# Kernel optimization log

Measured on AMD Instinct MI355X. Metric: run time of the kernel, lower is better.

## Reference

```python
import jax, jax.numpy as jnp
import numpy as np


def setup_inputs() -> dict:
    key = jax.random.key(0)
    ks = jax.random.split(key, 4)
    T, B, E = 2048, 2, 1024
    query = jax.random.normal(ks[0], (T, B, E), dtype=jnp.float32)
    attn_mask = jnp.zeros((T, T), dtype=jnp.float32)
    Wqkv = jax.random.normal(ks[1], (3 * E, E), dtype=jnp.float32) * 0.02
    bqkv = jnp.zeros((3 * E,), dtype=jnp.float32)
    Wout = jax.random.normal(ks[2], (E, E), dtype=jnp.float32) * 0.02
    bout = jnp.zeros((E,), dtype=jnp.float32)
    return {"query": query, "attn_mask": attn_mask, "Wqkv": Wqkv,
            "bqkv": bqkv, "Wout": Wout, "bout": bout, "num_heads": 16}


def reference(query, attn_mask, Wqkv, bqkv, Wout, bout, num_heads):
    T, B, E = query.shape
    H = num_heads
    hd = E // H
    scaling = hd ** -0.5
    # fused QKV projection: [T,B,3E]
    qkv = jnp.einsum('tbe,fe->tbf', query, Wqkv) + bqkv
    q, k, v = jnp.split(qkv, 3, axis=-1)
    q = q * scaling
    # [T,B,E] -> [B*H, T, hd]
    def to_heads(x):
        return x.reshape(T, B * H, hd).transpose(1, 0, 2)
    q, k, v = to_heads(q), to_heads(k), to_heads(v)
    # scores [B*H, T, T]
    scores = jnp.einsum('bth,bsh->bts', q, k) + attn_mask[None, :, :]
    probs = jax.nn.softmax(scores, axis=-1)  # dropout p=0
    attn = jnp.einsum('bts,bsh->bth', probs, v)  # [B*H, T, hd]
    attn = attn.transpose(1, 0, 2).reshape(T, B, E)
    out = jnp.einsum('tbe,fe->tbf', attn, Wout) + bout
    avg_w = probs.reshape(B, H, T, T).sum(axis=1) / H
    return out, avg_w
```

## Files before the change

### kernel.cpp

```cpp
#include <hip/hip_runtime.h>
#include <cstdint>
#include <cstddef>

#define Tt 2048
#define Bb 2
#define Ee 1024
#define Hh 16
#define HD 64
#define BHh (Bb*Hh)
#define Mm (Tt*Bb)

typedef short bf16x8 __attribute__((ext_vector_type(8)));
typedef float f32x4  __attribute__((ext_vector_type(4)));

#define MFMA16(a,b,c) __builtin_amdgcn_mfma_f32_16x16x32_bf16(a, b, c, 0, 0, 0)

__device__ __forceinline__ unsigned short f2bf(float f) {
    unsigned int u = __builtin_bit_cast(unsigned int, f);
    u += 0x7FFFu + ((u >> 16) & 1u);
    return (unsigned short)(u >> 16);
}
__device__ __forceinline__ unsigned int pack2bf(float lo, float hi) {
    return (unsigned int)f2bf(lo) | ((unsigned int)f2bf(hi) << 16);
}

__device__ __forceinline__ int swzA(int row, int dwcol) {
    return (row*32 + dwcol) ^ ((row & 7) << 2);
}
__device__ __forceinline__ int swzG(int row, int dwcol) {
    return (row*16 + dwcol) ^ ((row & 3) << 2);
}

__device__ __forceinline__ bf16x8 ldfrag(const unsigned short* base, int row, int col) {
    const unsigned int* p = (const unsigned int*)(base + row*66 + col);
    const unsigned int* q = (const unsigned int*)(base + row*66 + col + 16);
    uint4 u;
    u.x = p[0]; u.y = p[1];
    u.z = q[0]; u.w = q[1];
    return __builtin_bit_cast(bf16x8, u);
}

__global__ __launch_bounds__(256)
void to_bf16(const float* __restrict__ src, unsigned short* __restrict__ dst, int n8)
{
    const int stride = gridDim.x * 256;
    for (int i = blockIdx.x*256 + threadIdx.x; i < n8; i += stride) {
        const float4 a = ((const float4*)src)[2*i];
        const float4 b = ((const float4*)src)[2*i + 1];
        const uint4 u = {pack2bf(a.x,a.y), pack2bf(a.z,a.w),
                         pack2bf(b.x,b.y), pack2bf(b.z,b.w)};
        ((uint4*)dst)[i] = u;
    }
}

template<int MODE>
__global__ __launch_bounds__(256)
void gemm_mfma(const unsigned short* __restrict__ A, const unsigned short* __restrict__ W,
               const float* __restrict__ bias, float* __restrict__ Cout,
               unsigned short* __restrict__ qbuf, unsigned short* __restrict__ kbuf,
               unsigned short* __restrict__ vbuf, int N, int K)
{
    __shared__ __align__(16) unsigned int AsDW[2][128*16];
    __shared__ __align__(16) unsigned int WsDW[2][128*16];
    const int tid  = threadIdx.x;
    const int bm   = blockIdx.y * 128;
    const int bn   = blockIdx.x * 128;
    const int w    = tid >> 6;
    const int lane = tid & 63;
    const int lr   = lane & 15;
    const int lg   = lane >> 4;
    const int wm   = (w >> 1) * 64;
    const int wn   = (w & 1) * 64;

    f32x4 acc[4][4];
#pragma unroll
    for (int m = 0; m < 4; ++m)
#pragma unroll
        for (int n = 0; n < 4; ++n)
            acc[m][n] = f32x4{0.f, 0.f, 0.f, 0.f};

    const int r1  = tid >> 2;
    const int cdw = (tid & 3) * 4;

    {
        const uint4 a0 = *(const uint4*)&A[(size_t)(bm + r1)      * K + cdw*2];
        const uint4 a1 = *(const uint4*)&A[(size_t)(bm + r1 + 64) * K + cdw*2];
        const uint4 w0 = *(const uint4*)&W[(size_t)(bn + r1)      * K + cdw*2];
        const uint4 w1 = *(const uint4*)&W[(size_t)(bn + r1 + 64) * K + cdw*2];
        *(uint4*)(AsDW[0] + swzG(r1,      cdw)) = a0;
        *(uint4*)(AsDW[0] + swzG(r1 + 64, cdw)) = a1;
        *(uint4*)(WsDW[0] + swzG(r1,      cdw)) = w0;
        *(uint4*)(WsDW[0] + swzG(r1 + 64, cdw)) = w1;
        __syncthreads();
    }

    int cur = 0;
    for (int k0 = 0; k0 < K; k0 += 32) {
        const bool has_next = (k0 + 32 < K);
        uint4 an0, an1, wn0, wn1;
        if (has_next) {
            an0 = *(const uint4*)&A[(size_t)(bm + r1)      * K + k0 + 32 + cdw*2];
            an1 = *(const uint4*)&A[(size_t)(bm + r1 + 64) * K + k0 + 32 + cdw*2];
            wn0 = *(const uint4*)&W[(size_t)(bn + r1)      * K + k0 + 32 + cdw*2];
            wn1 = *(const uint4*)&W[(size_t)(bn + r1 + 64) * K + k0 + 32 + cdw*2];
        }

        const unsigned int* Ac = AsDW[cur];
        const unsigned int* Wc = WsDW[cur];
        bf16x8 af[4], wf[4];
#pragma unroll
        for (int i = 0; i < 4; ++i) {
            af[i] = __builtin_bit_cast(bf16x8, *(const uint4*)(Ac + swzG(wm + 16*i + lr, 4*lg)));
            wf[i] = __builtin_bit_cast(bf16x8, *(const uint4*)(Wc + swzG(wn + 16*i + lr, 4*lg)));
        }
#pragma unroll
        for (int m = 0; m < 4; ++m)
#pragma unroll
            for (int n = 0; n < 4; ++n)
                acc[m][n] = MFMA16(af[m], wf[n], acc[m][n]);

        if (has_next) {
            *(uint4*)(AsDW[cur ^ 1] + swzG(r1,      cdw)) = an0;
            *(uint4*)(AsDW[cur ^ 1] + swzG(r1 + 64, cdw)) = an1;
            *(uint4*)(WsDW[cur ^ 1] + swzG(r1,      cdw)) = wn0;
            *(uint4*)(WsDW[cur ^ 1] + swzG(r1 + 64, cdw)) = wn1;
        }
        __syncthreads();
        cur ^= 1;
    }

#pragma unroll
    for (int nsub = 0; nsub < 4; ++nsub) {
        const int n0 = bn + wn + 16*nsub + lr;
        const float bv = bias[n0];
#pragma unroll
        for (int msub = 0; msub < 4; ++msub) {
#pragma unroll
            for (int reg = 0; reg < 4; ++reg) {
                const int m = bm + wm + 16*msub + 4*lg + reg;
                float v = acc[msub][nsub][reg] + bv;
                if (MODE == 0) {
                    const int which = n0 >> 10;
                    const int e0 = n0 & 1023;
                    const int h = e0 >> 6, d0 = e0 & 63;
                    if (which == 0) v *= 0.125f;
                    unsigned short* dst = (which == 0) ? qbuf : (which == 1) ? kbuf : vbuf;
                    dst[((size_t)((m & 1)*Hh + h) * Tt + (m >> 1)) * HD + d0] = f2bf(v);
                } else {
                    Cout[(size_t)m * N + n0] = v;
                }
            }
        }
    }
}

__global__ __launch_bounds__(512)
void attn_mfma(const unsigned short* __restrict__ qb, const unsigned short* __restrict__ kb,
               const unsigned short* __restrict__ vb, const float* __restrict__ mask,
               unsigned short* __restrict__ attnb, float* __restrict__ lbuf)
{
    __shared__ __align__(16) unsigned int KsDW[2][64*32];
    __shared__ __align__(16) unsigned short Vt[2][64*66];
    __shared__ float l_sh[128];

    const int tid  = threadIdx.x;
    const int bid  = blockIdx.x;
    const int wid  = (bid & 7) * 64 + (bid >> 3);
    const int bh   = wid & 31;
    const int t0   = (wid >> 5) * 128;
    const int w    = tid >> 6;
    const int lane = tid & 63;
    const int lr   = lane & 15;
    const int lg   = lane >> 4;
    const int b = bh >> 4, h = bh & 15;

    const unsigned short* __restrict__ Qg = qb + (size_t)bh * Tt * HD;
    const unsigned short* __restrict__ Kg = kb + (size_t)bh * Tt * HD;
    const unsigned short* __restrict__ Vg = vb + (size_t)bh * Tt * HD;

    const int str = tid >> 3;
    const int sdw = (tid & 7) * 4;

    const int vdg = tid & 15;
    const int vs2 = tid >> 4;

    bf16x8 qf[2];
    for (int half = 0; half < 2; ++half) {
        __syncthreads();
        *(uint4*)(KsDW[0] + swzA(str, sdw)) =
            *(const uint4*)&Qg[(size_t)(t0 + half*64 + str) * HD + sdw*2];
        __syncthreads();
        if ((w >> 2) == half) {
            const int r = 16*(w & 3) + lr;
            qf[0] = __builtin_bit_cast(bf16x8, *(const uint4*)(KsDW[0] + swzA(r, 4*lg)));
            qf[1] = __builtin_bit_cast(bf16x8, *(const uint4*)(KsDW[0] + swzA(r, 16 + 4*lg)));
        }
    }

    f32x4 oacc[4];
#pragma unroll
    for (int d = 0; d < 4; ++d)
        oacc[d] = f32x4{0.f, 0.f, 0.f, 0.f};
    float lacc = 0.f;

    {
        const uint4 k0r = *(const uint4*)&Kg[(size_t)str * HD + sdw*2];
        const uint2 a0  = *(const uint2*)&Vg[(size_t)(2*vs2)     * HD + vdg*4];
        const uint2 c0  = *(const uint2*)&Vg[(size_t)(2*vs2 + 1) * HD + vdg*4];
        __syncthreads();
        *(uint4*)(KsDW[0] + swzA(str, sdw)) = k0r;
        unsigned short* vt0 = &Vt[0][0];
        *(unsigned int*)&vt0[(vdg*4+0)*66 + 2*vs2] = (a0.x & 0xFFFFu) | (c0.x << 16);
        *(unsigned int*)&vt0[(vdg*4+1)*66 + 2*vs2] = (a0.x >> 16)     | (c0.x & 0xFFFF0000u);
        *(unsigned int*)&vt0[(vdg*4+2)*66 + 2*vs2] = (a0.y & 0xFFFFu) | (c0.y << 16);
        *(unsigned int*)&vt0[(vdg*4+3)*66 + 2*vs2] = (a0.y >> 16)     | (c0.y & 0xFFFF0000u);
        __syncthreads();
    }

    int cur = 0;
    for (int s0 = 0; s0 < Tt; s0 += 64) {
        const bool has_next = (s0 + 64 < Tt);
        uint4 kn; uint2 van, vcn;
        if (has_next) {
            kn  = *(const uint4*)&Kg[(size_t)(s0 + 64 + str) * HD + sdw*2];
            van = *(const uint2*)&Vg[(size_t)(s0 + 64 + 2*vs2)     * HD + vdg*4];
            vcn = *(const uint2*)&Vg[(size_t)(s0 + 64 + 2*vs2 + 1) * HD + vdg*4];
        }

        const unsigned int* Kc = KsDW[cur];
        const unsigned short* Vc = &Vt[cur][0];

        f32x4 sacc[4];
#pragma unroll
        for (int ssub = 0; ssub < 4; ++ssub) {
            const bf16x8 a0 = __builtin_bit_cast(bf16x8,
                *(const uint4*)(Kc + swzA(16*ssub + lr, 4*lg)));
            const bf16x8 a1 = __builtin_bit_cast(bf16x8,
                *(const uint4*)(Kc + swzA(16*ssub + lr, 16 + 4*lg)));
            f32x4 z = {0.f, 0.f, 0.f, 0.f};
            z = MFMA16(a0, qf[0], z);
            z = MFMA16(a1, qf[1], z);
            sacc[ssub] = z;
        }

        unsigned int pw[8];
        {
            float lt = 0.f;
            const float* __restrict__ mrow =
                &mask[(size_t)(t0 + 16*w + lr) * Tt + s0];
#pragma unroll
            for (int ssub = 0; ssub < 4; ++ssub) {
                const float4 mv = *(const float4*)&mrow[16*ssub + 4*lg];
                const float e0 = __expf(sacc[ssub][0] + mv.x);
                const float e1 = __expf(sacc[ssub][1] + mv.y);
                const float e2 = __expf(sacc[ssub][2] + mv.z);
                const float e3 = __expf(sacc[ssub][3] + mv.w);
                lt += (e0 + e1) + (e2 + e3);
                pw[ssub*2]     = pack2bf(e0, e1);
                pw[ssub*2 + 1] = pack2bf(e2, e3);
            }
            lt += __shfl_xor(lt, 16);
            lt += __shfl_xor(lt, 32);
            lacc += lt;
        }

        const uint4 ua = {pw[0], pw[1], pw[2], pw[3]};
        const uint4 ub = {pw[4], pw[5], pw[6], pw[7]};
#pragma unroll
        for (int dsub = 0; dsub < 4; ++dsub) {
            const bf16x8 b0 = ldfrag(Vc, 16*dsub + lr, 4*lg);
            const bf16x8 b1 = ldfrag(Vc, 16*dsub + lr, 32 + 4*lg);
            oacc[dsub] = MFMA16(__builtin_bit_cast(bf16x8, ua), b0, oacc[dsub]);
            oacc[dsub] = MFMA16(__builtin_bit_cast(bf16x8, ub), b1, oacc[dsub]);
        }

        if (has_next) {
            *(uint4*)(KsDW[cur ^ 1] + swzA(str, sdw)) = kn;
            unsigned short* vt1 = &Vt[cur ^ 1][0];
            *(unsigned int*)&vt1[(vdg*4+0)*66 + 2*vs2] = (van.x & 0xFFFFu) | (vcn.x << 16);
            *(unsigned int*)&vt1[(vdg*4+1)*66 + 2*vs2] = (van.x >> 16)     | (vcn.x & 0xFFFF0000u);
            *(unsigned int*)&vt1[(vdg*4+2)*66 + 2*vs2] = (van.y & 0xFFFFu) | (vcn.y << 16);
            *(unsigned int*)&vt1[(vdg*4+3)*66 + 2*vs2] = (van.y >> 16)     | (vcn.y & 0xFFFF0000u);
        }
        __syncthreads();
        cur ^= 1;
    }

    if (lg == 0) l_sh[16*w + lr] = lacc;
    __syncthreads();
#pragma unroll
    for (int reg = 0; reg < 4; ++reg) {
        const int tl = 16*w + 4*lg + reg;
        const float inv = 1.f / l_sh[tl];
        const int t = t0 + tl;
#pragma unroll
        for (int dsub = 0; dsub < 4; ++dsub)
            attnb[((size_t)t * Bb + b) * Ee + h*HD + dsub*16 + lr] =
                f2bf(oacc[dsub][reg] * inv);
    }
    if (lg == 0)
        lbuf[(size_t)bh * Tt + t0 + 16*w + lr] = lacc;
}

__global__ __launch_bounds__(256)
void avg_probs_mfma(const unsigned short* __restrict__ qb, const unsigned short* __restrict__ kb,
                    const float* __restrict__ mask, const float* __restrict__ lbuf,
                    float* __restrict__ avg)
{
    __shared__ __align__(16) unsigned short Qs[2][64*66];
    __shared__ __align__(16) unsigned short Ksh[2][64*66];
    __shared__ float linv[16][64];

    const int tid  = threadIdx.x;
    const int b    = blockIdx.z;
    const int t0   = blockIdx.y * 64;
    const int s0   = blockIdx.x * 64;
    const int w    = tid >> 6;
    const int lane = tid & 63;
    const int lr   = lane & 15;
    const int lg   = lane >> 4;

    const int str = tid >> 2;
    const int stc = (tid & 3) * 16;

    {
        const int hh = tid >> 4, tl = (tid & 15) * 4;
        const float4 lv = *(const float4*)&lbuf[(size_t)(b*Hh + hh) * Tt + t0 + tl];
        linv[hh][tl+0] = 1.f / (16.f * lv.x);
        linv[hh][tl+1] = 1.f / (16.f * lv.y);
        linv[hh][tl+2] = 1.f / (16.f * lv.z);
        linv[hh][tl+3] = 1.f / (16.f * lv.w);

        const unsigned short* Qp = &qb[((size_t)(b*Hh) * Tt + t0 + str) * HD + stc];
        const unsigned short* Kp = &kb[((size_t)(b*Hh) * Tt + s0 + str) * HD + stc];
        const uint4 q0 = *(const uint4*)Qp;
        const uint4 q1 = *(const uint4*)(Qp + 8);
        const uint4 k0 = *(const uint4*)Kp;
        const uint4 k1 = *(const uint4*)(Kp + 8);
        *(uint4*)&Qs[0][str*66 + stc]      = q0;
        *(uint4*)&Qs[0][str*66 + stc + 8]  = q1;
        *(uint4*)&Ksh[0][str*66 + stc]     = k0;
        *(uint4*)&Ksh[0][str*66 + stc + 8] = k1;
        __syncthreads();
    }

    f32x4 mf[4];
#pragma unroll
    for (int ssub = 0; ssub < 4; ++ssub)
#pragma unroll
        for (int reg = 0; reg < 4; ++reg)
            mf[ssub][reg] = mask[(size_t)(t0 + 16*w + 4*lg + reg) * Tt + s0 + 16*ssub + lr];

    f32x4 av[4];
#pragma unroll
    for (int ssub = 0; ssub < 4; ++ssub) av[ssub] = f32x4{0.f, 0.f, 0.f, 0.f};

    int cur = 0;
    for (int h = 0; h < Hh; ++h) {
        const bool has_next = (h + 1 < Hh);
        uint4 qn0, qn1, kn0, kn1;
        if (has_next) {
            const unsigned short* Qp = &qb[((size_t)(b*Hh + h + 1) * Tt + t0 + str) * HD + stc];
            const unsigned short* Kp = &kb[((size_t)(b*Hh + h + 1) * Tt + s0 + str) * HD + stc];
            qn0 = *(const uint4*)Qp;
            qn1 = *(const uint4*)(Qp + 8);
            kn0 = *(const uint4*)Kp;
            kn1 = *(const uint4*)(Kp + 8);
        }

        const unsigned short* Qc = &Qs[cur][0];
        const unsigned short* Kc = &Ksh[cur][0];

        const float lv0 = linv[h][16*w + 4*lg + 0];
        const float lv1 = linv[h][16*w + 4*lg + 1];
        const float lv2 = linv[h][16*w + 4*lg + 2];
        const float lv3 = linv[h][16*w + 4*lg + 3];

        const bf16x8 af0 = ldfrag(Qc, 16*w + lr, 4*lg);
        const bf16x8 af1 = ldfrag(Qc, 16*w + lr, 32 + 4*lg);
#pragma unroll
        for (int ssub = 0; ssub < 4; ++ssub) {
            const bf16x8 bf0 = ldfrag(Kc, 16*ssub + lr, 4*lg);
            const bf16x8 bf1 = ldfrag(Kc, 16*ssub + lr, 32 + 4*lg);
            f32x4 z = {0.f, 0.f, 0.f, 0.f};
            z = MFMA16(af0, bf0, z);
            z = MFMA16(af1, bf1, z);
            av[ssub][0] += __expf(z[0] + mf[ssub][0]) * lv0;
            av[ssub][1] += __expf(z[1] + mf[ssub][1]) * lv1;
            av[ssub][2] += __expf(z[2] + mf[ssub][2]) * lv2;
            av[ssub][3] += __expf(z[3] + mf[ssub][3]) * lv3;
        }

        if (has_next) {
            *(uint4*)&Qs[cur ^ 1][str*66 + stc]      = qn0;
            *(uint4*)&Qs[cur ^ 1][str*66 + stc + 8]  = qn1;
            *(uint4*)&Ksh[cur ^ 1][str*66 + stc]     = kn0;
            *(uint4*)&Ksh[cur ^ 1][str*66 + stc + 8] = kn1;
        }
        __syncthreads();
        cur ^= 1;
    }

#pragma unroll
    for (int ssub = 0; ssub < 4; ++ssub)
#pragma unroll
        for (int reg = 0; reg < 4; ++reg)
            avg[((size_t)b * Tt + t0 + 16*w + 4*lg + reg) * Tt + s0 + 16*ssub + lr] =
                av[ssub][reg];
}

extern "C" void kernel_launch(void* const* d_in, const int* in_sizes, int n_in,
                              void* d_out, int out_size, void* d_ws, size_t ws_size,
                              hipStream_t stream)
{
    (void)in_sizes; (void)n_in; (void)out_size; (void)ws_size;
    const float* query = (const float*)d_in[0];
    const float* mask  = (const float*)d_in[1];
    const float* Wqkv  = (const float*)d_in[2];
    const float* bqkv  = (const float*)d_in[3];
    const float* Wout  = (const float*)d_in[4];
    const float* bout  = (const float*)d_in[5];

    float* out = (float*)d_out;
    float* avg = out + (size_t)Tt * Bb * Ee;

    const size_t S1 = (size_t)BHh * Tt * HD;
    unsigned short* wsu     = (unsigned short*)d_ws;
    unsigned short* qbuf    = wsu;
    unsigned short* kbuf    = qbuf + S1;
    unsigned short* vbuf    = kbuf + S1;
    unsigned short* attnb   = vbuf + S1;
    unsigned short* querybf = attnb + (size_t)Mm * Ee;
    unsigned short* wqkvbf  = querybf + (size_t)Mm * Ee;
    unsigned short* woutbf  = wqkvbf + (size_t)3 * Ee * Ee;
    float*          lbuf    = (float*)(woutbf + (size_t)Ee * Ee);

    to_bf16<<<1024, 256, 0, stream>>>(query, querybf, (Mm*Ee)/8);
    to_bf16<<<1024, 256, 0, stream>>>(Wqkv, wqkvbf, (3*Ee*Ee)/8);
    to_bf16<<<512,  256, 0, stream>>>(Wout, woutbf, (Ee*Ee)/8);

    gemm_mfma<0><<<dim3(3072/128, Mm/128), 256, 0, stream>>>(
        querybf, wqkvbf, bqkv, nullptr, qbuf, kbuf, vbuf, 3072, Ee);
    attn_mfma<<<dim3(BHh * (Tt/128)), 512, 0, stream>>>(
        qbuf, kbuf, vbuf, mask, attnb, lbuf);
    avg_probs_mfma<<<dim3(Tt/64, Tt/64, Bb), 256, 0, stream>>>(
        qbuf, kbuf, mask, lbuf, avg);
    gemm_mfma<1><<<dim3(Ee/128, Mm/128), 256, 0, stream>>>(
        attnb, woutbf, bout, out, nullptr, nullptr, nullptr, Ee, Ee);
}
```

Measured before the change: 198.6 us.

## Split attention over two key halves and merge partials in a reduce kernel

The attention kernel now splits the key/value sequence into two halves, doubling the number of blocks. Each block writes unnormalized fp32 partial outputs and row sums to workspace. A new reduce kernel adds the two halves, normalizes, converts to bf16 in the head-interleaved layout, and writes the combined row sums for the averaged-probability kernel. This aims for more parallelism and better CU occupancy, at the cost of an extra launch and substantial extra fp32 partial-result traffic.

```diff
diff --git a/kernel.cpp b/kernel.cpp
--- a/kernel.cpp
+++ b/kernel.cpp
@@ -157,22 +157,23 @@
 __global__ __launch_bounds__(512)
 void attn_mfma(const unsigned short* __restrict__ qb, const unsigned short* __restrict__ kb,
                const unsigned short* __restrict__ vb, const float* __restrict__ mask,
-               unsigned short* __restrict__ attnb, float* __restrict__ lbuf)
+               float* __restrict__ opart, float* __restrict__ lpart)
 {
     __shared__ __align__(16) unsigned int KsDW[2][64*32];
     __shared__ __align__(16) unsigned short Vt[2][64*66];
-    __shared__ float l_sh[128];
 
     const int tid  = threadIdx.x;
     const int bid  = blockIdx.x;
-    const int wid  = (bid & 7) * 64 + (bid >> 3);
+    const int wid  = (bid & 7) * 128 + (bid >> 3);
     const int bh   = wid & 31;
-    const int t0   = (wid >> 5) * 128;
+    const int r2   = wid >> 5;
+    const int t0   = (r2 >> 1) * 128;
+    const int sb   = (r2 & 1) * 1024;
+    const int half = r2 & 1;
     const int w    = tid >> 6;
     const int lane = tid & 63;
     const int lr   = lane & 15;
     const int lg   = lane >> 4;
-    const int b = bh >> 4, h = bh & 15;
 
     const unsigned short* __restrict__ Qg = qb + (size_t)bh * Tt * HD;
     const unsigned short* __restrict__ Kg = kb + (size_t)bh * Tt * HD;
@@ -185,12 +186,12 @@
     const int vs2 = tid >> 4;
 
     bf16x8 qf[2];
-    for (int half = 0; half < 2; ++half) {
+    for (int qh = 0; qh < 2; ++qh) {
         __syncthreads();
         *(uint4*)(KsDW[0] + swzA(str, sdw)) =
-            *(const uint4*)&Qg[(size_t)(t0 + half*64 + str) * HD + sdw*2];
-        __syncthreads();
-        if ((w >> 2) == half) {
+            *(const uint4*)&Qg[(size_t)(t0 + qh*64 + str) * HD + sdw*2];
+        __syncthreads();
+        if ((w >> 2) == qh) {
             const int r = 16*(w & 3) + lr;
             qf[0] = __builtin_bit_cast(bf16x8, *(const uint4*)(KsDW[0] + swzA(r, 4*lg)));
             qf[1] = __builtin_bit_cast(bf16x8, *(const uint4*)(KsDW[0] + swzA(r, 16 + 4*lg)));
@@ -204,9 +205,9 @@
     float lacc = 0.f;
 
     {
-        const uint4 k0r = *(const uint4*)&Kg[(size_t)str * HD + sdw*2];
-        const uint2 a0  = *(const uint2*)&Vg[(size_t)(2*vs2)     * HD + vdg*4];
-        const uint2 c0  = *(const uint2*)&Vg[(size_t)(2*vs2 + 1) * HD + vdg*4];
+        const uint4 k0r = *(const uint4*)&Kg[(size_t)(sb + str) * HD + sdw*2];
+        const uint2 a0  = *(const uint2*)&Vg[(size_t)(sb + 2*vs2)     * HD + vdg*4];
+        const uint2 c0  = *(const uint2*)&Vg[(size_t)(sb + 2*vs2 + 1) * HD + vdg*4];
         __syncthreads();
         *(uint4*)(KsDW[0] + swzA(str, sdw)) = k0r;
         unsigned short* vt0 = &Vt[0][0];
@@ -218,8 +219,8 @@
     }
 
     int cur = 0;
-    for (int s0 = 0; s0 < Tt; s0 += 64) {
-        const bool has_next = (s0 + 64 < Tt);
+    for (int s0 = sb; s0 < sb + 1024; s0 += 64) {
+        const bool has_next = (s0 + 64 < sb + 1024);
         uint4 kn; uint2 van, vcn;
         if (has_next) {
             kn  = *(const uint4*)&Kg[(size_t)(s0 + 64 + str) * HD + sdw*2];
@@ -286,20 +287,42 @@
         cur ^= 1;
     }
 
-    if (lg == 0) l_sh[16*w + lr] = lacc;
-    __syncthreads();
+    float* __restrict__ obase = opart + (size_t)(half*BHh + bh) * Tt * HD;
 #pragma unroll
     for (int reg = 0; reg < 4; ++reg) {
-        const int tl = 16*w + 4*lg + reg;
-        const float inv = 1.f / l_sh[tl];
-        const int t = t0 + tl;
+        const int t = t0 + 16*w + 4*lg + reg;
 #pragma unroll
         for (int dsub = 0; dsub < 4; ++dsub)
-            attnb[((size_t)t * Bb + b) * Ee + h*HD + dsub*16 + lr] =
-                f2bf(oacc[dsub][reg] * inv);
+            obase[(size_t)t * HD + dsub*16 + lr] = oacc[dsub][reg];
     }
     if (lg == 0)
-        lbuf[(size_t)bh * Tt + t0 + 16*w + lr] = lacc;
+        lpart[(size_t)half*BHh*Tt + (size_t)bh*Tt + t0 + 16*w + lr] = lacc;
+}
+
+__global__ __launch_bounds__(256)
+void attn_reduce(const float* __restrict__ opart, const float* __restrict__ lpart,
+                 unsigned short* __restrict__ attnb, float* __restrict__ lbuf)
+{
+    const int gid = blockIdx.x*256 + threadIdx.x;
+    const int row = gid >> 3;
+    const int c   = gid & 7;
+    const int bh  = row >> 11;
+    const int t   = row & 2047;
+    const float l = lpart[row] + lpart[(size_t)BHh*Tt + row];
+    const float inv = 1.f / l;
+    const size_t o0 = (size_t)row * HD + c*8;
+    const size_t o1 = (size_t)BHh * Tt * HD + o0;
+    const float4 a0 = *(const float4*)&opart[o0];
+    const float4 a1 = *(const float4*)&opart[o0 + 4];
+    const float4 b0 = *(const float4*)&opart[o1];
+    const float4 b1 = *(const float4*)&opart[o1 + 4];
+    const uint4 u = {
+        pack2bf((a0.x + b0.x)*inv, (a0.y + b0.y)*inv),
+        pack2bf((a0.z + b0.z)*inv, (a0.w + b0.w)*inv),
+        pack2bf((a1.x + b1.x)*inv, (a1.y + b1.y)*inv),
+        pack2bf((a1.z + b1.z)*inv, (a1.w + b1.w)*inv)};
+    *(uint4*)&attnb[((size_t)t * Bb + (bh >> 4)) * Ee + (bh & 15)*HD + c*8] = u;
+    if (c == 0) lbuf[row] = l;
 }
 
 __global__ __launch_bounds__(256)
@@ -434,6 +457,8 @@
     unsigned short* wqkvbf  = querybf + (size_t)Mm * Ee;
     unsigned short* woutbf  = wqkvbf + (size_t)3 * Ee * Ee;
     float*          lbuf    = (float*)(woutbf + (size_t)Ee * Ee);
+    float*          opart   = lbuf + (size_t)BHh * Tt;
+    float*          lpart   = opart + 2 * S1;
 
     to_bf16<<<1024, 256, 0, stream>>>(query, querybf, (Mm*Ee)/8);
     to_bf16<<<1024, 256, 0, stream>>>(Wqkv, wqkvbf, (3*Ee*Ee)/8);
@@ -441,8 +466,10 @@
 
     gemm_mfma<0><<<dim3(3072/128, Mm/128), 256, 0, stream>>>(
         querybf, wqkvbf, bqkv, nullptr, qbuf, kbuf, vbuf, 3072, Ee);
-    attn_mfma<<<dim3(BHh * (Tt/128)), 512, 0, stream>>>(
-        qbuf, kbuf, vbuf, mask, attnb, lbuf);
+    attn_mfma<<<dim3(BHh * (Tt/128) * 2), 512, 0, stream>>>(
+        qbuf, kbuf, vbuf, mask, opart, lpart);
+    attn_reduce<<<dim3((BHh*Tt*8)/256), 256, 0, stream>>>(
+        opart, lpart, attnb, lbuf);
     avg_probs_mfma<<<dim3(Tt/64, Tt/64, Bb), 256, 0, stream>>>(
         qbuf, kbuf, mask, lbuf, avg);
     gemm_mfma<1><<<dim3(Ee/128, Mm/128), 256, 0, stream>>>(
```

Result: slower. 214.0 us (+7.8%).
